# Performance work log

Hardware: AMD Instinct MI355X
Metric: run time of the kernel (lower is better)

## Reference

```python
import jax, jax.numpy as jnp
import numpy as np

D_EMBED = 1024
N_HEADS = 16


def setup_inputs() -> dict:
    key = jax.random.key(0)
    ks = jax.random.split(key, 5)
    x = jax.random.normal(ks[0], (4, 2048, D_EMBED), dtype=jnp.float32)
    # fused QKV projection: Linear(d, 3d)
    w_qkv = jax.random.normal(ks[1], (D_EMBED, 3 * D_EMBED), dtype=jnp.float32) / np.sqrt(D_EMBED)
    b_qkv = jnp.zeros((3 * D_EMBED,), dtype=jnp.float32)
    # output projection: Linear(d, d)
    w_o = jax.random.normal(ks[2], (D_EMBED, D_EMBED), dtype=jnp.float32) / np.sqrt(D_EMBED)
    b_o = jnp.zeros((D_EMBED,), dtype=jnp.float32)
    return {"x": x, "w_qkv": w_qkv, "b_qkv": b_qkv, "w_o": w_o, "b_o": b_o}


def reference(x, w_qkv, b_qkv, w_o, b_o):
    bs, sl, ed = x.shape
    nh = N_HEADS
    hd = ed // nh
    qkv = x @ w_qkv + b_qkv                      # [bs, sl, 3*ed]
    q, k, v = jnp.split(qkv, 3, axis=-1)
    # (bs, sl, nh*hd) -> (bs, nh, sl, hd)
    q = q.reshape(bs, sl, nh, hd).transpose(0, 2, 1, 3)
    k = k.reshape(bs, sl, nh, hd).transpose(0, 2, 1, 3)
    v = v.reshape(bs, sl, nh, hd).transpose(0, 2, 1, 3)
    att = jnp.einsum('bhqd,bhkd->bhqk', q, k) * (1.0 / np.sqrt(hd))
    causal = jnp.tril(jnp.ones((sl, sl), dtype=bool))
    att = jnp.where(causal[None, None], att, jnp.float32(-jnp.inf))
    att = jax.nn.softmax(att, axis=-1)
    y = jnp.einsum('bhqk,bhkd->bhqd', att, v)    # [bs, nh, sl, hd]
    y = y.transpose(0, 2, 1, 3).reshape(bs, sl, ed)
    return y @ w_o + b_o
```

## Files before the change

kernel.cpp:

```cpp
#include <hip/hip_runtime.h>
#include <hip/hip_bf16.h>
#include <stdint.h>

typedef __attribute__((ext_vector_type(8))) __bf16 bf16x8;
typedef __attribute__((ext_vector_type(4))) __bf16 bf16x4;
typedef __attribute__((ext_vector_type(4))) float f32x4;

#define MFMA16(a, b, c) __builtin_amdgcn_mfma_f32_16x16x32_bf16((a), (b), (c), 0, 0, 0)

static __device__ __forceinline__ void gload_lds16(const void* g, void* l) {
  __builtin_amdgcn_global_load_lds(
      reinterpret_cast<const __attribute__((address_space(1))) uint32_t*>(
          reinterpret_cast<uintptr_t>(g)),
      reinterpret_cast<__attribute__((address_space(3))) uint32_t*>(
          reinterpret_cast<uintptr_t>(l)),
      16, 0, 0);
}

__global__ __launch_bounds__(256) void prep_fused(
    const float* __restrict__ x, __bf16* __restrict__ xb,
    const float* __restrict__ wqkv, __bf16* __restrict__ wqkvT,
    const float* __restrict__ wo, __bf16* __restrict__ woT) {
  __shared__ float tile[32][33];
  const int bid = (int)blockIdx.x;
  const int tid = threadIdx.x;
  if (bid < 4096) {
    int i = bid * 2048 + tid * 8;
    float4 a = *(const float4*)(x + i);
    float4 b = *(const float4*)(x + i + 4);
    bf16x8 o;
    o[0] = (__bf16)a.x; o[1] = (__bf16)a.y; o[2] = (__bf16)a.z; o[3] = (__bf16)a.w;
    o[4] = (__bf16)b.x; o[5] = (__bf16)b.y; o[6] = (__bf16)b.z; o[7] = (__bf16)b.w;
    *(bf16x8*)(xb + i) = o;
    return;
  }
  const float* in;
  __bf16* out;
  int C, bx, by;
  if (bid < 7168) {
    int t = bid - 4096;
    in = wqkv; out = wqkvT; C = 3072;
    bx = t % 96; by = t / 96;
  } else {
    int t = bid - 7168;
    in = wo; out = woT; C = 1024;
    bx = t & 31; by = t >> 5;
  }
  const int R = 1024;
  int tx = tid & 31, ty = tid >> 5;
  int c0 = bx * 32, r0 = by * 32;
#pragma unroll
  for (int i = 0; i < 4; i++)
    tile[ty + i * 8][tx] = in[(size_t)(r0 + ty + i * 8) * C + c0 + tx];
  __syncthreads();
#pragma unroll
  for (int i = 0; i < 4; i++)
    out[(size_t)(c0 + ty + i * 8) * R + r0 + tx] = (__bf16)tile[tx][ty + i * 8];
}

template <int EPI, int NPAN>
__global__ __launch_bounds__(512) void gemm_pipe(
    const __bf16* __restrict__ A, const __bf16* __restrict__ Bt,
    const float* __restrict__ bias, float* __restrict__ Cf,
    __bf16* __restrict__ Qb, __bf16* __restrict__ Kb, __bf16* __restrict__ Vtb, int N) {
  __shared__ __bf16 lA[3][128 * 32];
  __shared__ __bf16 lB[3][256 * 32];
  const int bid0 = (int)blockIdx.x;
  const int tM = (bid0 & 7) * 8 + ((bid0 >> 3) & 7);
  const int tN0 = bid0 >> 6;
  const int tid = threadIdx.x;
  const int w = tid >> 6, lane = tid & 63;
  const int wr = w >> 2, wc = w & 3;
  const int lr = lane & 15, lg = lane >> 4;

  const int srow = tid >> 2;
  const int gcol = ((tid & 3) ^ ((tid >> 3) & 3)) * 8;
  const __bf16* Asrc = A + (size_t)(tM * 128 + srow) * 1024 + gcol;
  const int aslot = (lg ^ ((lr >> 1) & 3)) * 8;

#pragma unroll 1
  for (int p = 0; p < NPAN; ++p) {
    const int tN = tN0 + p * 4;
    const __bf16* Bsrc0 = Bt + (size_t)(tN * 256 + srow) * 1024 + gcol;
    const __bf16* Bsrc1 = Bt + (size_t)(tN * 256 + 128 + srow) * 1024 + gcol;

    f32x4 acc[4][4];
#pragma unroll
    for (int m = 0; m < 4; m++)
#pragma unroll
      for (int n = 0; n < 4; n++) acc[m][n] = f32x4{0.f, 0.f, 0.f, 0.f};

    auto stage = [&](int slot, int t) {
      const int k0 = t * 32;
      gload_lds16(Asrc + k0, &lA[slot][tid * 8]);
      gload_lds16(Bsrc0 + k0, &lB[slot][tid * 8]);
      gload_lds16(Bsrc1 + k0, &lB[slot][4096 + tid * 8]);
    };
    auto compute = [&](int slot) {
      bf16x8 a[4], b[4];
#pragma unroll
      for (int m = 0; m < 4; m++) {
        int row = wr * 64 + m * 16 + lr;
        a[m] = *(const bf16x8*)&lA[slot][row * 32 + aslot];
      }
#pragma unroll
      for (int n = 0; n < 4; n++) {
        int row = wc * 64 + n * 16 + lr;
        b[n] = *(const bf16x8*)&lB[slot][row * 32 + aslot];
      }
      __builtin_amdgcn_s_setprio(1);
#pragma unroll
      for (int m = 0; m < 4; m++)
#pragma unroll
        for (int n = 0; n < 4; n++) acc[m][n] = MFMA16(a[m], b[n], acc[m][n]);
      __builtin_amdgcn_s_setprio(0);
    };

    stage(0, 0); stage(1, 1);
    asm volatile("s_waitcnt vmcnt(3)" ::: "memory");
    __builtin_amdgcn_s_barrier();

#pragma unroll 1
    for (int t = 0; t < 30; ++t) {
      stage((t + 2) % 3, t + 2);
      compute(t % 3);
      asm volatile("s_waitcnt vmcnt(3)" ::: "memory");
      __builtin_amdgcn_s_barrier();
    }
    compute(30 % 3);
    asm volatile("s_waitcnt vmcnt(0)" ::: "memory");
    __builtin_amdgcn_s_barrier();
    compute(31 % 3);

#pragma unroll
    for (int m = 0; m < 4; m++) {
#pragma unroll
      for (int n = 0; n < 4; n++) {
        int row0 = tM * 128 + wr * 64 + m * 16 + lg * 4;
        int col = tN * 256 + wc * 64 + n * 16 + lr;
        float bv = bias[col];
        if (EPI == 0) {
          int which = col >> 10, rem = col & 1023;
          int hh = rem >> 6, dd = rem & 63;
          if (which == 2) {
#pragma unroll
            for (int r = 0; r < 4; r++) {
              int row = row0 + r;
              int b = row >> 11, s = row & 2047;
              Vtb[((size_t)(b * 16 + hh) * 64 + dd) * 2048 + s] = (__bf16)(acc[m][n][r] + bv);
            }
          } else {
            __bf16* dst = (which == 0) ? Qb : Kb;
            float sc = (which == 0) ? 0.18033688f : 1.0f;
#pragma unroll
            for (int r = 0; r < 4; r++) {
              int row = row0 + r;
              int b = row >> 11, s = row & 2047;
              dst[((size_t)(b * 16 + hh) * 2048 + s) * 64 + dd] = (__bf16)((acc[m][n][r] + bv) * sc);
            }
          }
        } else {
#pragma unroll
          for (int r = 0; r < 4; r++)
            Cf[(size_t)(row0 + r) * N + col] = acc[m][n][r] + bv;
        }
      }
    }
    if (p + 1 < NPAN) __syncthreads();
  }
}

__global__ __launch_bounds__(512) void attn_fwd(
    const __bf16* __restrict__ Q, const __bf16* __restrict__ K,
    const __bf16* __restrict__ Vt, __bf16* __restrict__ Y) {
  const int pair = blockIdx.y;
  const int bh = blockIdx.x;
  const int w = threadIdx.x >> 6, lane = threadIdx.x & 63;
  const int lr = lane & 15, lg = lane >> 4;
  const int b = bh >> 4, h = bh & 15;
  const __bf16* Qp = Q + (size_t)bh * 131072;
  const __bf16* Kp = K + (size_t)bh * 131072;
  const __bf16* Vp = Vt + (size_t)bh * 131072;

  __shared__ __bf16 Kl[4][4096];
  __shared__ __bf16 Vl[4][4096];
  __shared__ __bf16 Pl[8][16 * 64];
  __bf16* Pw = Pl[w];

  bf16x8 kones;
#pragma unroll
  for (int j = 0; j < 8; j++) kones[j] = (__bf16)1.0f;

  auto stage = [&](int slot, int t_) {
    const int kv0_ = t_ * 64;
    int rr = w * 8 + (lane >> 3);
    int sc = ((lane & 7) ^ (rr & 7)) * 8;
    gload_lds16(Kp + (size_t)(kv0_ + rr) * 64 + sc, &Kl[slot][w * 512]);
    gload_lds16(Vp + (size_t)rr * 2048 + kv0_ + sc, &Vl[slot][w * 512]);
  };

  for (int sel = 0; sel < 2; ++sel) {
    const int qt = sel ? (15 - pair) : pair;
    const int qbase = qt * 128 + w * 16;

    bf16x8 aq[2];
#pragma unroll
    for (int c = 0; c < 2; c++)
      aq[c] = *(const bf16x8*)&Qp[(size_t)(qbase + lr) * 64 + c * 32 + lg * 8];

    f32x4 acc_o[4];
    f32x4 acc_l;
#pragma unroll
    for (int dn = 0; dn < 4; dn++) acc_o[dn] = f32x4{0.f, 0.f, 0.f, 0.f};
    acc_l = f32x4{0.f, 0.f, 0.f, 0.f};

    const int nt = 2 * qt + 2;

    stage(0, 0);
    stage(1, 1);

#pragma unroll 1
    for (int t = 0; t < nt; ++t) {
      const int kv0 = t * 64;
      if (t + 2 < nt) stage((t + 2) & 3, t + 2);

      if (t + 2 < nt) {
        asm volatile("s_waitcnt vmcnt(4)" ::: "memory");
      } else if (t + 1 < nt) {
        asm volatile("s_waitcnt vmcnt(2)" ::: "memory");
      } else {
        asm volatile("s_waitcnt vmcnt(0)" ::: "memory");
      }
      __builtin_amdgcn_s_barrier();

      if (kv0 <= qbase + 15) {
        const int cur = t & 3;
        f32x4 s4[4];
#pragma unroll
        for (int n = 0; n < 4; n++) s4[n] = f32x4{0.f, 0.f, 0.f, 0.f};
        __builtin_amdgcn_s_setprio(1);
#pragma unroll
        for (int c = 0; c < 2; c++) {
#pragma unroll
          for (int n = 0; n < 4; n++) {
            int kr = n * 16 + lr;
            int off = kr * 64 + (((c * 64 + lg * 16) ^ ((kr & 7) << 4)) >> 1);
            bf16x8 bk = *(const bf16x8*)&Kl[cur][off];
            s4[n] = MFMA16(bk, aq[c], s4[n]);
          }
        }
        __builtin_amdgcn_s_setprio(0);

        const bool diag = (kv0 + 63 > qbase);
        const int qrow = qbase + lr;
        if (diag) {
#pragma unroll
          for (int n = 0; n < 4; n++)
#pragma unroll
            for (int r = 0; r < 4; r++)
              if (kv0 + n * 16 + lg * 4 + r > qrow) s4[n][r] = -1e30f;
        }
#pragma unroll
        for (int n = 0; n < 4; n++) {
          bf16x4 pq;
#pragma unroll
          for (int r = 0; r < 4; r++)
            pq[r] = (__bf16)__builtin_amdgcn_exp2f(s4[n][r] - 16.0f);
          int off = lr * 64 + (((n * 32 + lg * 8) ^ ((lr & 7) << 4)) >> 1);
          *(bf16x4*)&Pw[off] = pq;
        }

        bf16x8 ap[2];
#pragma unroll
        for (int cc = 0; cc < 2; cc++) {
          int off = lr * 64 + (((cc * 64 + lg * 16) ^ ((lr & 7) << 4)) >> 1);
          ap[cc] = *(const bf16x8*)&Pw[off];
        }

        __builtin_amdgcn_s_setprio(1);
#pragma unroll
        for (int cc = 0; cc < 2; cc++)
          acc_l = MFMA16(ap[cc], kones, acc_l);
#pragma unroll
        for (int dn = 0; dn < 4; dn++) {
          int d = dn * 16 + lr;
#pragma unroll
          for (int cc = 0; cc < 2; cc++) {
            int off = d * 64 + (((cc * 64 + lg * 16) ^ ((d & 7) << 4)) >> 1);
            bf16x8 bv = *(const bf16x8*)&Vl[cur][off];
            acc_o[dn] = MFMA16(ap[cc], bv, acc_o[dn]);
          }
        }
        __builtin_amdgcn_s_setprio(0);
      }
    }

    __syncthreads();

#pragma unroll
    for (int r = 0; r < 4; r++) {
      float iv = 1.f / acc_l[r];
      int row = b * 2048 + qbase + lg * 4 + r;
#pragma unroll
      for (int dn = 0; dn < 4; dn++)
        Y[(size_t)row * 1024 + h * 64 + dn * 16 + lr] = (__bf16)(acc_o[dn][r] * iv);
    }
  }
}

extern "C" void kernel_launch(void* const* d_in, const int* in_sizes, int n_in,
                              void* d_out, int out_size, void* d_ws, size_t ws_size,
                              hipStream_t stream) {
  const float* x = (const float*)d_in[0];
  const float* wqkv = (const float*)d_in[1];
  const float* bqkv = (const float*)d_in[2];
  const float* wo = (const float*)d_in[3];
  const float* bo = (const float*)d_in[4];
  float* out = (float*)d_out;

  __bf16* ws = (__bf16*)d_ws;
  __bf16* xb = ws;
  __bf16* wqkvT = xb + 8388608;
  __bf16* woT = wqkvT + 3145728;
  __bf16* Qb = woT + 1048576;
  __bf16* Kb = Qb + 8388608;
  __bf16* Vtb = Kb + 8388608;
  __bf16* Yb = xb;

  prep_fused<<<8192, 256, 0, stream>>>(x, xb, wqkv, wqkvT, wo, woT);
  gemm_pipe<0, 3><<<256, 512, 0, stream>>>(xb, wqkvT, bqkv, nullptr, Qb, Kb, Vtb, 3072);
  attn_fwd<<<dim3(64, 8), 512, 0, stream>>>(Qb, Kb, Vtb, Yb);
  gemm_pipe<1, 1><<<256, 512, 0, stream>>>(Yb, woT, bo, out, nullptr, nullptr, nullptr, 1024);
}
```

Measured before the change: 146.8 us.

## Prefetch next GEMM panel during tail compute and vectorize V-transpose stores

The multi-panel GEMM loop now issues the first two K-stage loads of the next N panel during the last two compute steps of the current panel. It rotates the triple-buffer slot offset across panels instead of refilling the pipeline, which removes the per-panel prologue stall and the trailing __syncthreads. The V^T epilogue also writes four consecutive sequence positions as one bf16x4 store instead of four scalar stores. The cost is more complex slot indexing. The vector store assumes row0 is 4-aligned, which holds given lg*4.

```diff
diff --git a/kernel.cpp b/kernel.cpp
--- a/kernel.cpp
+++ b/kernel.cpp
@@ -78,11 +78,15 @@
   const __bf16* Asrc = A + (size_t)(tM * 128 + srow) * 1024 + gcol;
   const int aslot = (lg ^ ((lr >> 1) & 3)) * 8;
 
+  int off = 0;
 #pragma unroll 1
   for (int p = 0; p < NPAN; ++p) {
     const int tN = tN0 + p * 4;
     const __bf16* Bsrc0 = Bt + (size_t)(tN * 256 + srow) * 1024 + gcol;
     const __bf16* Bsrc1 = Bt + (size_t)(tN * 256 + 128 + srow) * 1024 + gcol;
+    const int tNn = tN0 + (p + 1) * 4;
+    const __bf16* Bn0 = Bt + (size_t)(tNn * 256 + srow) * 1024 + gcol;
+    const __bf16* Bn1 = Bt + (size_t)(tNn * 256 + 128 + srow) * 1024 + gcol;
 
     f32x4 acc[4][4];
 #pragma unroll
@@ -96,6 +100,12 @@
       gload_lds16(Bsrc0 + k0, &lB[slot][tid * 8]);
       gload_lds16(Bsrc1 + k0, &lB[slot][4096 + tid * 8]);
     };
+    auto stageN = [&](int slot, int t) {
+      const int k0 = t * 32;
+      gload_lds16(Asrc + k0, &lA[slot][tid * 8]);
+      gload_lds16(Bn0 + k0, &lB[slot][tid * 8]);
+      gload_lds16(Bn1 + k0, &lB[slot][4096 + tid * 8]);
+    };
     auto compute = [&](int slot) {
       bf16x8 a[4], b[4];
 #pragma unroll
@@ -116,21 +126,33 @@
       __builtin_amdgcn_s_setprio(0);
     };
 
-    stage(0, 0); stage(1, 1);
-    asm volatile("s_waitcnt vmcnt(3)" ::: "memory");
-    __builtin_amdgcn_s_barrier();
+    if (p == 0) {
+      stage(0, 0); stage(1, 1);
+      asm volatile("s_waitcnt vmcnt(3)" ::: "memory");
+      __builtin_amdgcn_s_barrier();
+    }
 
 #pragma unroll 1
     for (int t = 0; t < 30; ++t) {
-      stage((t + 2) % 3, t + 2);
-      compute(t % 3);
+      stage((t + 2 + off) % 3, t + 2);
+      compute((t + off) % 3);
       asm volatile("s_waitcnt vmcnt(3)" ::: "memory");
       __builtin_amdgcn_s_barrier();
     }
-    compute(30 % 3);
-    asm volatile("s_waitcnt vmcnt(0)" ::: "memory");
+    compute((30 + off) % 3);
+    if (p + 1 < NPAN) {
+      stageN((32 + off) % 3, 0);
+      asm volatile("s_waitcnt vmcnt(3)" ::: "memory");
+    } else {
+      asm volatile("s_waitcnt vmcnt(0)" ::: "memory");
+    }
     __builtin_amdgcn_s_barrier();
-    compute(31 % 3);
+    compute((31 + off) % 3);
+    if (p + 1 < NPAN) {
+      stageN((33 + off) % 3, 1);
+      asm volatile("s_waitcnt vmcnt(3)" ::: "memory");
+      __builtin_amdgcn_s_barrier();
+    }
 
 #pragma unroll
     for (int m = 0; m < 4; m++) {
@@ -143,12 +165,11 @@
           int which = col >> 10, rem = col & 1023;
           int hh = rem >> 6, dd = rem & 63;
           if (which == 2) {
-#pragma unroll
-            for (int r = 0; r < 4; r++) {
-              int row = row0 + r;
-              int b = row >> 11, s = row & 2047;
-              Vtb[((size_t)(b * 16 + hh) * 64 + dd) * 2048 + s] = (__bf16)(acc[m][n][r] + bv);
-            }
+            int bb = row0 >> 11, s0 = row0 & 2047;
+            bf16x4 v;
+#pragma unroll
+            for (int r = 0; r < 4; r++) v[r] = (__bf16)(acc[m][n][r] + bv);
+            *(bf16x4*)&Vtb[((size_t)(bb * 16 + hh) * 64 + dd) * 2048 + s0] = v;
           } else {
             __bf16* dst = (which == 0) ? Qb : Kb;
             float sc = (which == 0) ? 0.18033688f : 1.0f;
@@ -166,7 +187,7 @@
         }
       }
     }
-    if (p + 1 < NPAN) __syncthreads();
+    off = (off + 2) % 3;
   }
 }
 
```

Result: no change. 147.3 us (+0.3%).

## Replace QKV GEMM with 256x384 tile double-buffered kernel

Applied to the files above, without the earlier changes.

Adds a new QKV projection kernel that computes a 256x384 output tile per block, up from the 128x256 panels used before, with two LDS buffers and an 8x6 MFMA accumulator grid per wave. Each staged A and B fragment feeds more MFMAs, which raises arithmetic intensity and cuts LDS and global traffic per FLOP. The cost is much higher register pressure (192 accumulator floats per lane), which can limit occupancy or cause spills. Pipelining depth also drops from three stages to two.

```diff
diff --git a/kernel.cpp b/kernel.cpp
--- a/kernel.cpp
+++ b/kernel.cpp
@@ -58,6 +58,104 @@
     out[(size_t)(c0 + ty + i * 8) * R + r0 + tx] = (__bf16)tile[tx][ty + i * 8];
 }
 
+__global__ __launch_bounds__(512) void gemm_fat(
+    const __bf16* __restrict__ A, const __bf16* __restrict__ Bt,
+    const float* __restrict__ bias,
+    __bf16* __restrict__ Qb, __bf16* __restrict__ Kb, __bf16* __restrict__ Vtb) {
+  __shared__ __bf16 lA[2][8192];
+  __shared__ __bf16 lB[2][12288];
+  const int bid0 = (int)blockIdx.x;
+  const int tM = (bid0 & 7) * 4 + ((bid0 >> 3) & 3);
+  const int tN = bid0 >> 5;
+  const int tid = threadIdx.x;
+  const int w = tid >> 6, lane = tid & 63;
+  const int wr = w >> 2, wc = w & 3;
+  const int lr = lane & 15, lg = lane >> 4;
+
+  const int srow = tid >> 2;
+  const int gcol = ((tid & 3) ^ ((tid >> 3) & 3)) * 8;
+  const __bf16* Asrc = A + (size_t)(tM * 256 + srow) * 1024 + gcol;
+  const __bf16* Bsrc = Bt + (size_t)(tN * 384 + srow) * 1024 + gcol;
+
+  f32x4 acc[8][6];
+#pragma unroll
+  for (int m = 0; m < 8; m++)
+#pragma unroll
+    for (int n = 0; n < 6; n++) acc[m][n] = f32x4{0.f, 0.f, 0.f, 0.f};
+
+  auto stage = [&](int slot, int t) {
+    const int k0 = t * 32;
+    gload_lds16(Asrc + k0, &lA[slot][tid * 8]);
+    gload_lds16(Asrc + 128 * 1024 + k0, &lA[slot][4096 + tid * 8]);
+    gload_lds16(Bsrc + k0, &lB[slot][tid * 8]);
+    gload_lds16(Bsrc + 128 * 1024 + k0, &lB[slot][4096 + tid * 8]);
+    gload_lds16(Bsrc + 256 * 1024 + k0, &lB[slot][8192 + tid * 8]);
+  };
+
+  const int aslot = (lg ^ ((lr >> 1) & 3)) * 8;
+  auto compute = [&](int slot) {
+    bf16x8 bfr[6];
+#pragma unroll
+    for (int n = 0; n < 6; n++) {
+      int row = wc * 96 + n * 16 + lr;
+      bfr[n] = *(const bf16x8*)&lB[slot][row * 32 + aslot];
+    }
+    __builtin_amdgcn_s_setprio(1);
+#pragma unroll
+    for (int m = 0; m < 8; m++) {
+      int row = wr * 128 + m * 16 + lr;
+      bf16x8 a = *(const bf16x8*)&lA[slot][row * 32 + aslot];
+#pragma unroll
+      for (int n = 0; n < 6; n++) acc[m][n] = MFMA16(a, bfr[n], acc[m][n]);
+    }
+    __builtin_amdgcn_s_setprio(0);
+  };
+
+  stage(0, 0);
+  int cur = 0;
+#pragma unroll 1
+  for (int t = 0; t < 32; ++t) {
+    __builtin_amdgcn_s_barrier();
+    if (t + 1 < 32) {
+      stage(cur ^ 1, t + 1);
+      asm volatile("s_waitcnt vmcnt(5)" ::: "memory");
+    } else {
+      asm volatile("s_waitcnt vmcnt(0)" ::: "memory");
+    }
+    __builtin_amdgcn_s_barrier();
+    compute(cur);
+    cur ^= 1;
+  }
+
+#pragma unroll
+  for (int m = 0; m < 8; m++) {
+#pragma unroll
+    for (int n = 0; n < 6; n++) {
+      int row0 = tM * 256 + wr * 128 + m * 16 + lg * 4;
+      int col = tN * 384 + wc * 96 + n * 16 + lr;
+      float bv = bias[col];
+      int which = col >> 10, rem = col & 1023;
+      int hh = rem >> 6, dd = rem & 63;
+      if (which == 2) {
+        int bb = row0 >> 11, s0 = row0 & 2047;
+        bf16x4 v;
+#pragma unroll
+        for (int r = 0; r < 4; r++) v[r] = (__bf16)(acc[m][n][r] + bv);
+        *(bf16x4*)&Vtb[((size_t)(bb * 16 + hh) * 64 + dd) * 2048 + s0] = v;
+      } else {
+        __bf16* dst = (which == 0) ? Qb : Kb;
+        float sc = (which == 0) ? 0.18033688f : 1.0f;
+#pragma unroll
+        for (int r = 0; r < 4; r++) {
+          int row = row0 + r;
+          int b = row >> 11, s = row & 2047;
+          dst[((size_t)(b * 16 + hh) * 2048 + s) * 64 + dd] = (__bf16)((acc[m][n][r] + bv) * sc);
+        }
+      }
+    }
+  }
+}
+
 template <int EPI, int NPAN>
 __global__ __launch_bounds__(512) void gemm_pipe(
     const __bf16* __restrict__ A, const __bf16* __restrict__ Bt,
@@ -328,7 +426,7 @@
   __bf16* Yb = xb;
 
   prep_fused<<<8192, 256, 0, stream>>>(x, xb, wqkv, wqkvT, wo, woT);
-  gemm_pipe<0, 3><<<256, 512, 0, stream>>>(xb, wqkvT, bqkv, nullptr, Qb, Kb, Vtb, 3072);
+  gemm_fat<<<256, 512, 0, stream>>>(xb, wqkvT, bqkv, Qb, Kb, Vtb);
   attn_fwd<<<dim3(64, 8), 512, 0, stream>>>(Qb, Kb, Vtb, Yb);
   gemm_pipe<1, 1><<<256, 512, 0, stream>>>(Yb, woT, bo, out, nullptr, nullptr, nullptr, 1024);
 }
```

Measured after the change: 142.1 us, median of 2. 3.2% less time.
